# Performance work log

Hardware: AMD Instinct MI355X
Metric: run time of the kernel (lower is better)

Reference implementation:

```python
import jax, jax.numpy as jnp
import numpy as np

N_EXPERT_CAPACITY = 2  # init kwarg; k = S * capacity // E


def setup_inputs() -> dict:
    key = jax.random.key(0)
    k1, k2, k3, k4 = jax.random.split(key, 4)
    B, S, D, E, F = 8, 1024, 1024, 8, 2048
    # kaiming-uniform-ish scales
    x = jax.random.normal(k1, (B, S, D), dtype=jnp.float32)
    choice_w = jax.random.uniform(k2, (E, D), dtype=jnp.float32, minval=-1.0, maxval=1.0) * (1.0 / np.sqrt(D))
    w1 = jax.random.uniform(k3, (E, D, F), dtype=jnp.float32, minval=-1.0, maxval=1.0) * (1.0 / np.sqrt(D))
    w2 = jax.random.uniform(k4, (E, F, D), dtype=jnp.float32, minval=-1.0, maxval=1.0) * (1.0 / np.sqrt(F))
    return {"x": x, "choice_w": choice_w, "w1": w1, "w2": w2}


def reference(x, choice_w, w1, w2):
    B, S, D = x.shape
    E = choice_w.shape[0]
    k = S * N_EXPERT_CAPACITY // E  # tokens per expert (expert-choice)
    # router softmax over experts: [B, S, E]
    probs = jax.nn.softmax(jnp.einsum('bsd,ed->bse', x, choice_w), axis=-1)
    # each expert picks its top-k tokens: G, I are [B, E, k]
    G, I = jax.lax.top_k(jnp.swapaxes(probs, -1, -2), k)
    # dispatch: gather tokens instead of one-hot matmul (same math)
    x_in = jnp.take_along_axis(x[:, None, :, :], I[..., None], axis=2)  # [B, E, k, D]
    # per-expert MLP with SiLU
    h = jax.nn.silu(jnp.einsum('bekd,edf->bekf', x_in, w1))  # [B, E, k, F]
    x_mlp = jnp.einsum('bekf,efd->bekd', h, w2)              # [B, E, k, D]
    # combine: weighted scatter-add back to token positions (equals P,G,x_mlp einsum)
    b_idx = jnp.arange(B)[:, None, None]  # [B,1,1] broadcasts with I [B,E,k]
    out = jnp.zeros_like(x).at[b_idx, I].add(G[..., None] * x_mlp)
    return out
```

## Files before the change

kernel.cpp:

```cpp
#include <hip/hip_runtime.h>
#include <hip/hip_bf16.h>
#include <math.h>

#define B_   8
#define S_   1024
#define D_   1024
#define E_   8
#define F_   2048
#define KCAP 256

typedef __bf16 bf16x8 __attribute__((ext_vector_type(8)));
typedef float  floatx4 __attribute__((ext_vector_type(4)));
typedef unsigned short ushortx8 __attribute__((ext_vector_type(8)));

__device__ __forceinline__ unsigned short f2b(float f) {
    union { float f; unsigned int u; } v; v.f = f;
    unsigned int u = v.u;
    u += 0x7fffu + ((u >> 16) & 1u);
    return (unsigned short)(u >> 16);
}
__device__ __forceinline__ float b2f(unsigned short u) {
    union { unsigned int u; float f; } v; v.u = ((unsigned)u) << 16; return v.f;
}

__device__ __forceinline__ void gl_lds16(const void* g, void* l) {
    __builtin_amdgcn_global_load_lds(
        (const __attribute__((address_space(1))) void*)g,
        (__attribute__((address_space(3))) void*)l, 16, 0, 0);
}

__device__ __forceinline__ unsigned long long topk_key(float p, int s) {
    return (((unsigned long long)__float_as_uint(p)) << 10) | (unsigned)(S_ - 1 - s);
}

__global__ void router_kernel(const float* __restrict__ x, const float* __restrict__ cw,
                              float* __restrict__ probs, unsigned short* __restrict__ xb) {
    int gid  = blockIdx.x * 256 + threadIdx.x;
    int wave = gid >> 6;
    int lane = gid & 63;
    int b = wave >> 10;
    int s = wave & (S_ - 1);
    const float* xrow = x + ((size_t)b * S_ + s) * D_;
    unsigned short* xbrow = xb + ((size_t)b * S_ + s) * D_;
    float acc[E_];
#pragma unroll
    for (int e = 0; e < E_; e++) acc[e] = 0.f;
#pragma unroll
    for (int it = 0; it < D_ / 256; it++) {
        int i = it * 256 + lane * 4;
        float4 xv = *(const float4*)(xrow + i);
        ushort4 o;
        o.x = f2b(xv.x); o.y = f2b(xv.y); o.z = f2b(xv.z); o.w = f2b(xv.w);
        *(ushort4*)(xbrow + i) = o;
#pragma unroll
        for (int e = 0; e < E_; e++) {
            float4 wv = *(const float4*)(cw + e * D_ + i);
            acc[e] = fmaf(xv.x, wv.x, fmaf(xv.y, wv.y, fmaf(xv.z, wv.z, fmaf(xv.w, wv.w, acc[e]))));
        }
    }
#pragma unroll
    for (int e = 0; e < E_; e++) {
        float v = acc[e];
#pragma unroll
        for (int off = 32; off >= 1; off >>= 1) v += __shfl_down(v, off, 64);
        acc[e] = v;
    }
    if (lane == 0) {
        float m = acc[0];
#pragma unroll
        for (int e = 1; e < E_; e++) m = fmaxf(m, acc[e]);
        float sum = 0.f;
#pragma unroll
        for (int e = 0; e < E_; e++) { acc[e] = __expf(acc[e] - m); sum += acc[e]; }
        float inv = 1.f / sum;
#pragma unroll
        for (int e = 0; e < E_; e++) probs[((size_t)b * E_ + e) * S_ + s] = acc[e] * inv;
    }
}

union PrepSm {
    float tile[128][33];
    unsigned long long keys[S_];
};
__global__ void prep_kernel(const float* __restrict__ w1, const float* __restrict__ w2,
                            unsigned short* __restrict__ w1t, unsigned short* __restrict__ w2t,
                            const float* __restrict__ probs, int* __restrict__ I,
                            float* __restrict__ G, unsigned short* __restrict__ Pmap) {
    const int bid = blockIdx.x;
    const int tid = threadIdx.x;
    __shared__ PrepSm sm;

    if (bid >= 2 * 4096) {
        const int be = bid - 2 * 4096;
        const int b = be >> 3, e = be & 7;
        const float* rowp = probs + (size_t)be * S_;
#pragma unroll
        for (int q = 0; q < 4; q++) {
            const int s = q * 256 + tid;
            sm.keys[s] = topk_key(rowp[s], s);
            Pmap[((size_t)(b * S_ + s)) * E_ + e] = 0;
        }
        __syncthreads();
        unsigned long long my[4];
        int r[4] = {0, 0, 0, 0};
#pragma unroll
        for (int q = 0; q < 4; q++) my[q] = sm.keys[q * 256 + tid];
#pragma unroll 8
        for (int t = 0; t < S_; t++) {
            const unsigned long long kt = sm.keys[t];
#pragma unroll
            for (int q = 0; q < 4; q++) r[q] += (kt > my[q]);
        }
#pragma unroll
        for (int q = 0; q < 4; q++) {
            if (r[q] < KCAP) {
                const int s = q * 256 + tid;
                I[be * KCAP + r[q]] = s;
                G[be * KCAP + r[q]] = rowp[s];
                Pmap[((size_t)(b * S_ + s)) * E_ + e] = (unsigned short)(r[q] + 1);
            }
        }
        return;
    }

    const float* in;
    unsigned short* out;
    int R, C, e, c0, r0;
    if (bid < 4096) {
        in = w1; out = w1t; R = D_; C = F_;
        e = bid >> 9;
        const int t = bid & 511;
        c0 = (t & 63) * 32; r0 = (t >> 6) * 128;
    } else {
        const int b2 = bid - 4096;
        in = w2; out = w2t; R = F_; C = D_;
        e = b2 >> 9;
        const int t = b2 & 511;
        c0 = (t & 31) * 32; r0 = (t >> 5) * 128;
    }
    const float* ine = in + (size_t)e * R * C;
    unsigned short* oute = out + (size_t)e * R * C;

    const int lrow = tid >> 3;
    const int seg  = tid & 7;
    float4 v[4];
#pragma unroll
    for (int i = 0; i < 4; i++)
        v[i] = *(const float4*)(ine + (size_t)(r0 + lrow + i * 32) * C + c0 + seg * 4);
#pragma unroll
    for (int i = 0; i < 4; i++) {
        const int rr = lrow + i * 32;
        sm.tile[rr][seg * 4 + 0] = v[i].x; sm.tile[rr][seg * 4 + 1] = v[i].y;
        sm.tile[rr][seg * 4 + 2] = v[i].z; sm.tile[rr][seg * 4 + 3] = v[i].w;
    }
    __syncthreads();

    const int c = tid >> 3;
    const int k = tid & 7;
#pragma unroll
    for (int srep = 0; srep < 2; srep++) {
        const int s8 = k + srep * 8;
        ushortx8 o;
#pragma unroll
        for (int j = 0; j < 8; j++) o[j] = f2b(sm.tile[s8 * 8 + j][c]);
        *(ushortx8*)(oute + (size_t)(c0 + c) * R + r0 + s8 * 8) = o;
    }
}


__global__ __launch_bounds__(256, 4) void gemm1_kernel(
    const unsigned short* __restrict__ xb,
    const unsigned short* __restrict__ w1t,
    const int* __restrict__ I,
    unsigned short* __restrict__ H)
{
    const int g  = blockIdx.x;
    const int e  = g & 7;
    const int rr = g >> 3;
    const int b  = rr >> 5;
    const int t5 = rr & 31;
    const int be = b * 8 + e;
    const int mt = t5 & 1;
    const int nt = t5 >> 1;
    const int tid = threadIdx.x;

    __shared__ __align__(16) unsigned short Asm[128 * 64];
    __shared__ __align__(16) unsigned short Bsm[128 * 64];
    __shared__ unsigned int ArowS[128];

    if (tid < 128) {
        int tok = I[(size_t)be * KCAP + mt * 128 + tid];
        ArowS[tid] = (unsigned)((b * S_ + tok) * D_);
    }
    __syncthreads();

    const int r8   = tid >> 3;
    const int kseg = (tid & 7) ^ (r8 & 7);
    unsigned aoffW[4];
#pragma unroll
    for (int w = 0; w < 4; w++) aoffW[w] = ArowS[w * 32 + r8] + kseg * 8;
    const size_t boff0 = ((size_t)e * F_ + nt * 128 + r8) * D_ + kseg * 8;

    const int lane = tid & 63;
    const int wv   = tid >> 6;
    const int wm   = (wv & 1) * 64;
    const int wn   = (wv >> 1) * 64;
    const int l15  = lane & 15;
    const int quad = lane >> 4;
    const int x0   = (quad ^ (l15 & 7)) * 8;

    int aoffs[4], boffs[4];
#pragma unroll
    for (int i = 0; i < 4; i++) {
        aoffs[i] = (wm + i * 16 + l15) * 64 + x0;
        boffs[i] = (wn + i * 16 + l15) * 64 + x0;
    }

    floatx4 acc[4][4];
#pragma unroll
    for (int i = 0; i < 4; i++)
#pragma unroll
        for (int j = 0; j < 4; j++) acc[i][j] = (floatx4){0.f, 0.f, 0.f, 0.f};

    for (int k0 = 0; k0 < D_; k0 += 64) {
#pragma unroll
        for (int w = 0; w < 4; w++) {
            gl_lds16(xb  + aoffW[w] + k0,                    &Asm[(w * 256 + tid) * 8]);
            gl_lds16(w1t + boff0 + (size_t)w * 32 * D_ + k0, &Bsm[(w * 256 + tid) * 8]);
        }
        __syncthreads();
        bf16x8 af[4], bfr[4];
#pragma unroll
        for (int i = 0; i < 4; i++) {
            af[i]  = *(const bf16x8*)&Asm[aoffs[i]];
            bfr[i] = *(const bf16x8*)&Bsm[boffs[i]];
        }
#pragma unroll
        for (int i = 0; i < 4; i++)
#pragma unroll
            for (int j = 0; j < 4; j++)
                acc[i][j] = __builtin_amdgcn_mfma_f32_16x16x32_bf16(af[i], bfr[j], acc[i][j], 0, 0, 0);
#pragma unroll
        for (int i = 0; i < 4; i++) {
            af[i]  = *(const bf16x8*)&Asm[aoffs[i] ^ 32];
            bfr[i] = *(const bf16x8*)&Bsm[boffs[i] ^ 32];
        }
#pragma unroll
        for (int i = 0; i < 4; i++)
#pragma unroll
            for (int j = 0; j < 4; j++)
                acc[i][j] = __builtin_amdgcn_mfma_f32_16x16x32_bf16(af[i], bfr[j], acc[i][j], 0, 0, 0);
        __syncthreads();
    }

    unsigned short* Hbe = H + (size_t)be * KCAP * F_;
#pragma unroll
    for (int i = 0; i < 4; i++) {
#pragma unroll
        for (int r = 0; r < 4; r++) {
            int m = mt * 128 + wm + i * 16 + quad * 4 + r;
            unsigned short* hrow = Hbe + (size_t)m * F_ + nt * 128;
#pragma unroll
            for (int j = 0; j < 4; j++) {
                float v = acc[i][j][r];
                float sv = v / (1.f + __expf(-v));
                hrow[wn + j * 16 + l15] = f2b(sv);
            }
        }
    }
}

__global__ __launch_bounds__(256, 4) void gemm2_kernel(
    const unsigned short* __restrict__ H,
    const unsigned short* __restrict__ w2t,
    unsigned short* __restrict__ xmlp)
{
    const int g  = blockIdx.x;
    const int e  = g & 7;
    const int rr = g >> 3;
    const int b  = rr >> 4;
    const int t4 = rr & 15;
    const int be = b * 8 + e;
    const int mt = t4 & 1;
    const int nt = t4 >> 1;
    const int tid = threadIdx.x;

    __shared__ __align__(16) unsigned short Asm2[128 * 64];
    __shared__ __align__(16) unsigned short Bsm2[128 * 64];

    const int r8   = tid >> 3;
    const int kseg = (tid & 7) ^ (r8 & 7);
    const size_t aoff0 = ((size_t)be * KCAP + mt * 128 + r8) * F_ + kseg * 8;
    const size_t boff0 = ((size_t)e * D_ + nt * 128 + r8) * F_ + kseg * 8;

    const int lane = tid & 63;
    const int wv   = tid >> 6;
    const int wm   = (wv & 1) * 64;
    const int wn   = (wv >> 1) * 64;
    const int l15  = lane & 15;
    const int quad = lane >> 4;
    const int x0   = (quad ^ (l15 & 7)) * 8;

    int aoffs[4], boffs[4];
#pragma unroll
    for (int i = 0; i < 4; i++) {
        aoffs[i] = (wm + i * 16 + l15) * 64 + x0;
        boffs[i] = (wn + i * 16 + l15) * 64 + x0;
    }

    floatx4 acc[4][4];
#pragma unroll
    for (int i = 0; i < 4; i++)
#pragma unroll
        for (int j = 0; j < 4; j++) acc[i][j] = (floatx4){0.f, 0.f, 0.f, 0.f};

    for (int k0 = 0; k0 < F_; k0 += 64) {
#pragma unroll
        for (int w = 0; w < 4; w++) {
            gl_lds16(H   + aoff0 + (size_t)w * 32 * F_ + k0, &Asm2[(w * 256 + tid) * 8]);
            gl_lds16(w2t + boff0 + (size_t)w * 32 * F_ + k0, &Bsm2[(w * 256 + tid) * 8]);
        }
        __syncthreads();
        bf16x8 af[4], bfr[4];
#pragma unroll
        for (int i = 0; i < 4; i++) {
            af[i]  = *(const bf16x8*)&Asm2[aoffs[i]];
            bfr[i] = *(const bf16x8*)&Bsm2[boffs[i]];
        }
#pragma unroll
        for (int i = 0; i < 4; i++)
#pragma unroll
            for (int j = 0; j < 4; j++)
                acc[i][j] = __builtin_amdgcn_mfma_f32_16x16x32_bf16(af[i], bfr[j], acc[i][j], 0, 0, 0);
#pragma unroll
        for (int i = 0; i < 4; i++) {
            af[i]  = *(const bf16x8*)&Asm2[aoffs[i] ^ 32];
            bfr[i] = *(const bf16x8*)&Bsm2[boffs[i] ^ 32];
        }
#pragma unroll
        for (int i = 0; i < 4; i++)
#pragma unroll
            for (int j = 0; j < 4; j++)
                acc[i][j] = __builtin_amdgcn_mfma_f32_16x16x32_bf16(af[i], bfr[j], acc[i][j], 0, 0, 0);
        __syncthreads();
    }

    unsigned short* Xbe = xmlp + (size_t)be * KCAP * D_;
#pragma unroll
    for (int i = 0; i < 4; i++) {
#pragma unroll
        for (int r = 0; r < 4; r++) {
            int m = mt * 128 + wm + i * 16 + quad * 4 + r;
            unsigned short* orow = Xbe + (size_t)m * D_ + nt * 128;
#pragma unroll
            for (int j = 0; j < 4; j++)
                orow[wn + j * 16 + l15] = f2b(acc[i][j][r]);
        }
    }
}

__global__ void combine_kernel(const unsigned short* __restrict__ xmlp,
                               const unsigned short* __restrict__ Pmap,
                               const float* __restrict__ G,
                               float* __restrict__ out) {
    int gid  = blockIdx.x * 256 + threadIdx.x;
    int wave = gid >> 6;
    int lane = gid & 63;
    int b = wave >> 10;
    float acc[16];
#pragma unroll
    for (int i = 0; i < 16; i++) acc[i] = 0.f;
    const unsigned short* pm = Pmap + (size_t)wave * E_;
#pragma unroll
    for (int e = 0; e < E_; e++) {
        int pe = pm[e];
        if (pe) {
            int beslot = (b * E_ + e) * KCAP + (pe - 1);
            float g = G[beslot];
            const unsigned short* rw = xmlp + (size_t)beslot * D_ + lane * 16;
            ushortx8 r0 = *(const ushortx8*)(rw);
            ushortx8 r1 = *(const ushortx8*)(rw + 8);
#pragma unroll
            for (int i = 0; i < 8; i++) {
                acc[i]     = fmaf(g, b2f(r0[i]), acc[i]);
                acc[8 + i] = fmaf(g, b2f(r1[i]), acc[8 + i]);
            }
        }
    }
    float* orow = out + (size_t)wave * D_ + lane * 16;
    ((float4*)orow)[0] = make_float4(acc[0],  acc[1],  acc[2],  acc[3]);
    ((float4*)orow)[1] = make_float4(acc[4],  acc[5],  acc[6],  acc[7]);
    ((float4*)orow)[2] = make_float4(acc[8],  acc[9],  acc[10], acc[11]);
    ((float4*)orow)[3] = make_float4(acc[12], acc[13], acc[14], acc[15]);
}

extern "C" void kernel_launch(void* const* d_in, const int* in_sizes, int n_in,
                              void* d_out, int out_size, void* d_ws, size_t ws_size,
                              hipStream_t stream) {
    const float* x  = (const float*)d_in[0];
    const float* cw = (const float*)d_in[1];
    const float* w1 = (const float*)d_in[2];
    const float* w2 = (const float*)d_in[3];
    float* out = (float*)d_out;

    char* ws = (char*)d_ws;
    float*          probs = (float*)(ws);
    int*            Ibuf  = (int*)(ws + 262144);
    float*          Gbuf  = (float*)(ws + 327680);
    unsigned short* Pmap  = (unsigned short*)(ws + 393216);
    unsigned short* xb    = (unsigned short*)(ws + 524288);
    unsigned short* w1t   = (unsigned short*)(ws + 17301504);
    unsigned short* xmlp  = w1t;
    unsigned short* w2t   = (unsigned short*)(ws + 50855936);
    unsigned short* Hbuf  = (unsigned short*)(ws + 84410368);

    router_kernel<<<(B_ * S_ * 64) / 256, 256, 0, stream>>>(x, cw, probs, xb);
    prep_kernel<<<2 * 4096 + B_ * E_, 256, 0, stream>>>(w1, w2, w1t, w2t, probs, Ibuf, Gbuf, Pmap);
    gemm1_kernel<<<B_ * E_ * 2 * (F_ / 128), 256, 0, stream>>>(xb, w1t, Ibuf, Hbuf);
    gemm2_kernel<<<B_ * E_ * 2 * (D_ / 128), 256, 0, stream>>>(Hbuf, w2t, xmlp);
    combine_kernel<<<(B_ * S_ * 64) / 256, 256, 0, stream>>>(xmlp, Pmap, Gbuf, out);
}
```

Baseline: 381.8 us.

## Make weight transpose persistent with double-buffered LDS and prefetched tiles

The weight-transpose part of the prep kernel now runs as 768 persistent blocks that loop over the 8192 tiles, instead of one block per tile. Each iteration prefetches the next tile's global loads into registers while the current tile is converted and written out, using a double-buffered LDS tile and a single barrier per iteration. The top-k blocks move to the front of the grid so they start early. This aims to hide global load latency and cut block launch overhead, but it lowers the number of resident blocks and relies on manual waitcnt and barrier handling.

```diff
diff --git a/kernel.cpp b/kernel.cpp
--- a/kernel.cpp
+++ b/kernel.cpp
@@ -79,9 +79,24 @@
 }
 
 union PrepSm {
-    float tile[128][33];
+    float tile[2][128][33];
     unsigned long long keys[S_];
 };
+
+#define PREP_DECODE(T, INP, OUTP, RV, CV, C0, R0) do { \
+    int t_ = (T); \
+    if (t_ < 4096) { \
+        int e_ = t_ >> 9, tt_ = t_ & 511; \
+        INP = w1 + (size_t)e_ * D_ * F_;  OUTP = w1t + (size_t)e_ * D_ * F_; \
+        RV = D_; CV = F_; C0 = (tt_ & 63) * 32; R0 = (tt_ >> 6) * 128; \
+    } else { \
+        int t2_ = t_ - 4096; \
+        int e_ = t2_ >> 9, tt_ = t2_ & 511; \
+        INP = w2 + (size_t)e_ * D_ * F_;  OUTP = w2t + (size_t)e_ * D_ * F_; \
+        RV = F_; CV = D_; C0 = (tt_ & 31) * 32; R0 = (tt_ >> 5) * 128; \
+    } \
+} while (0)
+
 __global__ void prep_kernel(const float* __restrict__ w1, const float* __restrict__ w2,
                             unsigned short* __restrict__ w1t, unsigned short* __restrict__ w2t,
                             const float* __restrict__ probs, int* __restrict__ I,
@@ -90,8 +105,8 @@
     const int tid = threadIdx.x;
     __shared__ PrepSm sm;
 
-    if (bid >= 2 * 4096) {
-        const int be = bid - 2 * 4096;
+    if (bid < B_ * E_) {
+        const int be = bid;
         const int b = be >> 3, e = be & 7;
         const float* rowp = probs + (size_t)be * S_;
 #pragma unroll
@@ -123,47 +138,51 @@
         return;
     }
 
-    const float* in;
-    unsigned short* out;
-    int R, C, e, c0, r0;
-    if (bid < 4096) {
-        in = w1; out = w1t; R = D_; C = F_;
-        e = bid >> 9;
-        const int t = bid & 511;
-        c0 = (t & 63) * 32; r0 = (t >> 6) * 128;
-    } else {
-        const int b2 = bid - 4096;
-        in = w2; out = w2t; R = F_; C = D_;
-        e = b2 >> 9;
-        const int t = b2 & 511;
-        c0 = (t & 31) * 32; r0 = (t >> 5) * 128;
-    }
-    const float* ine = in + (size_t)e * R * C;
-    unsigned short* oute = out + (size_t)e * R * C;
-
+    const int tb   = bid - B_ * E_;
     const int lrow = tid >> 3;
     const int seg  = tid & 7;
+    const int c    = tid >> 3;
+    const int k    = tid & 7;
+
+    const float* inp; unsigned short* outp; int R, C, c0, r0;
+    PREP_DECODE(tb, inp, outp, R, C, c0, r0);
     float4 v[4];
 #pragma unroll
     for (int i = 0; i < 4; i++)
-        v[i] = *(const float4*)(ine + (size_t)(r0 + lrow + i * 32) * C + c0 + seg * 4);
-#pragma unroll
-    for (int i = 0; i < 4; i++) {
-        const int rr = lrow + i * 32;
-        sm.tile[rr][seg * 4 + 0] = v[i].x; sm.tile[rr][seg * 4 + 1] = v[i].y;
-        sm.tile[rr][seg * 4 + 2] = v[i].z; sm.tile[rr][seg * 4 + 3] = v[i].w;
-    }
-    __syncthreads();
-
-    const int c = tid >> 3;
-    const int k = tid & 7;
-#pragma unroll
-    for (int srep = 0; srep < 2; srep++) {
-        const int s8 = k + srep * 8;
-        ushortx8 o;
-#pragma unroll
-        for (int j = 0; j < 8; j++) o[j] = f2b(sm.tile[s8 * 8 + j][c]);
-        *(ushortx8*)(oute + (size_t)(c0 + c) * R + r0 + s8 * 8) = o;
+        v[i] = *(const float4*)(inp + (size_t)(r0 + lrow + i * 32) * C + c0 + seg * 4);
+
+    int buf = 0;
+    for (int T = tb; T < 8192; T += 768) {
+        unsigned short* oute = outp;
+        const int Rr = R, cc0 = c0, rr0 = r0;
+
+#pragma unroll
+        for (int i = 0; i < 4; i++) {
+            const int rr = lrow + i * 32;
+            sm.tile[buf][rr][seg * 4 + 0] = v[i].x;
+            sm.tile[buf][rr][seg * 4 + 1] = v[i].y;
+            sm.tile[buf][rr][seg * 4 + 2] = v[i].z;
+            sm.tile[buf][rr][seg * 4 + 3] = v[i].w;
+        }
+        if (T + 768 < 8192) {
+            PREP_DECODE(T + 768, inp, outp, R, C, c0, r0);
+#pragma unroll
+            for (int i = 0; i < 4; i++)
+                v[i] = *(const float4*)(inp + (size_t)(r0 + lrow + i * 32) * C + c0 + seg * 4);
+        }
+        __builtin_amdgcn_sched_barrier(0);
+        asm volatile("s_waitcnt lgkmcnt(0)" ::: "memory");
+        __builtin_amdgcn_s_barrier();
+        __builtin_amdgcn_sched_barrier(0);
+#pragma unroll
+        for (int srep = 0; srep < 2; srep++) {
+            const int s8 = k + srep * 8;
+            ushortx8 o;
+#pragma unroll
+            for (int j = 0; j < 8; j++) o[j] = f2b(sm.tile[buf][s8 * 8 + j][c]);
+            *(ushortx8*)(oute + (size_t)(cc0 + c) * Rr + rr0 + s8 * 8) = o;
+        }
+        buf ^= 1;
     }
 }
 
@@ -415,7 +434,7 @@
     unsigned short* Hbuf  = (unsigned short*)(ws + 84410368);
 
     router_kernel<<<(B_ * S_ * 64) / 256, 256, 0, stream>>>(x, cw, probs, xb);
-    prep_kernel<<<2 * 4096 + B_ * E_, 256, 0, stream>>>(w1, w2, w1t, w2t, probs, Ibuf, Gbuf, Pmap);
+    prep_kernel<<<B_ * E_ + 768, 256, 0, stream>>>(w1, w2, w1t, w2t, probs, Ibuf, Gbuf, Pmap);
     gemm1_kernel<<<B_ * E_ * 2 * (F_ / 128), 256, 0, stream>>>(xb, w1t, Ibuf, Hbuf);
     gemm2_kernel<<<B_ * E_ * 2 * (D_ / 128), 256, 0, stream>>>(Hbuf, w2t, xmlp);
     combine_kernel<<<(B_ * S_ * 64) / 256, 256, 0, stream>>>(xmlp, Pmap, Gbuf, out);
```

New measurement: 355.4 us, median of 2. 6.9% less time.
